# Kernel optimization log

Hardware: AMD Instinct MI355X
Metric: run time of the kernel (lower is better)

The kernel has to match this reference:

```python
import jax, jax.numpy as jnp
import numpy as np

EPS = 1e-16  # PyG softmax denominator epsilon


def segment_softmax(alpha, batch, num_segments):
    # alpha: (n,1); softmax within each bag (PyG-style: subtract segment max)
    m = jax.ops.segment_max(alpha, batch, num_segments=num_segments)
    e = jnp.exp(alpha - m[batch])
    s = jax.ops.segment_sum(e, batch, num_segments=num_segments)
    return e / (s[batch] + EPS)


def global_softmax_pooling(x, alpha, batch, num_segments):
    a = segment_softmax(alpha, batch, num_segments)
    return jax.ops.segment_sum(x * a, batch, num_segments=num_segments)  # (B,d)


def setup_inputs() -> dict:
    key = jax.random.key(0)
    k1, k2 = jax.random.split(key)
    n, d, B = 262144, 256, 512
    x = jax.random.normal(k1, (n, d), dtype=jnp.float32)
    batch = jnp.sort(jax.random.randint(k2, (n,), 0, B))
    return {"x": x, "batch": batch, "num_segments": B}


def reference(x, batch, num_segments):
    K = 3  # module default k
    alpha = jnp.zeros((x.shape[0], 1), dtype=x.dtype)
    for _ in range(K):  # small fixed iteration count
        z = global_softmax_pooling(x, alpha, batch, num_segments)  # (B,d)
        energy = jnp.sum(z * z, axis=1, keepdims=True)  # (B,1)
        z_squashed = jnp.sqrt(energy) / (1.0 + energy) * z  # (B,d)
        # alpha_i += <x_i, z_squashed[batch_i]> (vectorizes the per-bag mm loop)
        alpha = alpha + jnp.sum(x * z_squashed[batch], axis=1, keepdims=True)
    return global_softmax_pooling(x, alpha, batch, num_segments)
```

## Files before the change

### kernel.cpp

```cpp
#include <hip/hip_runtime.h>

#define D 256
#define CPS 4
#define TPB0 256
#define TPB1 1024
#define SLOTS 32
#define PSTR (D + 1)

__device__ __forceinline__ unsigned bfbits(float f) {
    unsigned u = __float_as_uint(f);
    return (u + 0x7fffu + ((u >> 16) & 1u)) >> 16;
}
__device__ __forceinline__ float bflo(unsigned u) { return __uint_as_float(u << 16); }
__device__ __forceinline__ float bfhi(unsigned u) { return __uint_as_float(u & 0xffff0000u); }

template<int USE_WS>
__global__ __launch_bounds__(TPB0, 8)
void pass0_k(const float* __restrict__ x, unsigned short* __restrict__ xb,
             const int* __restrict__ batch, float* __restrict__ part_out, int n)
{
    __shared__ float zp[8][D];
    __shared__ float sp[8];
    __shared__ int bnd[2];
    const int tid = threadIdx.x;
    const int s = blockIdx.x / CPS, k = blockIdx.x % CPS;
    const int hw = tid >> 5, l = tid & 31;

    if (tid < 2) {
        const int key = s + tid;
        int lo = 0, hi = n;
        while (lo < hi) { int mid = (lo + hi) >> 1; if (batch[mid] < key) lo = mid + 1; else hi = mid; }
        bnd[tid] = lo;
    }
    __syncthreads();
    const int start = bnd[0];
    const int cnt   = bnd[1] - start;
    const int csz   = (cnt + CPS - 1) / CPS;
    const int rbeg  = k * csz;
    const int rend  = min(cnt, rbeg + csz);

    float za[8] = {0,0,0,0,0,0,0,0};
    float s_acc = 0.f;
#pragma unroll 2
    for (int r = rbeg + hw; r < rend; r += 8) {
        const size_t boff = (size_t)(start + r) * D + l * 8;
        const float4 v0 = *(const float4*)(x + boff);
        const float4 v1 = *(const float4*)(x + boff + 4);
        if (USE_WS) {
            uint4 p;
            p.x = bfbits(v0.x) | (bfbits(v0.y) << 16);
            p.y = bfbits(v0.z) | (bfbits(v0.w) << 16);
            p.z = bfbits(v1.x) | (bfbits(v1.y) << 16);
            p.w = bfbits(v1.z) | (bfbits(v1.w) << 16);
            *(uint4*)(xb + boff) = p;
        }
        s_acc += 1.f;
        za[0] += v0.x; za[1] += v0.y; za[2] += v0.z; za[3] += v0.w;
        za[4] += v1.x; za[5] += v1.y; za[6] += v1.z; za[7] += v1.w;
    }
#pragma unroll
    for (int j = 0; j < 8; ++j) zp[hw][l * 8 + j] = za[j];
    if (l == 0) sp[hw] = s_acc;
    __syncthreads();
    float acc = 0.f;
#pragma unroll
    for (int h = 0; h < 8; ++h) acc += zp[h][tid];
    float* po = part_out + (size_t)(s * CPS + k) * PSTR;
    po[tid] = acc;
    if (tid == 0) {
        float st = 0.f;
#pragma unroll
        for (int h = 0; h < 8; ++h) st += sp[h];
        po[D] = st;
    }
}

template<int USE_WS>
__global__ __launch_bounds__(TPB1, 8)
void phases_k(const float* __restrict__ x, const unsigned short* __restrict__ xb,
              const int* __restrict__ batch,
              const float* __restrict__ part, float* __restrict__ out, int n)
{
    __shared__ float zp[SLOTS][D];
    __shared__ float sp[SLOTS];
    __shared__ float zs[D];
    __shared__ float red_e[16];
    __shared__ float red[2];
    __shared__ int bnd[2];
    const int tid  = threadIdx.x;
    const int s    = blockIdx.x;
    const int slot = tid >> 5;
    const int l    = tid & 31;
    const int wv   = tid >> 6;

    if (tid < 2) {
        const int key = s + tid;
        int lo = 0, hi = n;
        while (lo < hi) { int mid = (lo + hi) >> 1; if (batch[mid] < key) lo = mid + 1; else hi = mid; }
        bnd[tid] = lo;
    }
    __syncthreads();
    const int start = bnd[0];
    const int cnt   = bnd[1] - start;

    const float* pb = part + (size_t)s * CPS * PSTR;
    float z = 0.f;
    if (tid < D) {
#pragma unroll
        for (int kk = 0; kk < CPS; ++kk) z += pb[kk * PSTR + tid];
    }
    if (tid == 0) {
        float st = 0.f;
#pragma unroll
        for (int kk = 0; kk < CPS; ++kk) st += pb[kk * PSTR + D];
        red[0] = 1.f / (st + 1e-16f);
    }
    __syncthreads();
    z *= red[0];

    float Scol = 0.f;
    float zr[8];

    for (int ph = 1; ph <= 3; ++ph) {
        float e = (tid < D) ? z * z : 0.f;
#pragma unroll
        for (int o = 32; o; o >>= 1) e += __shfl_xor(e, o);
        if ((tid & 63) == 0) red_e[wv] = e;
        __syncthreads();
        if (tid == 0) {
            float E = 0.f;
#pragma unroll
            for (int h = 0; h < 16; ++h) E += red_e[h];
            red[1] = (E > 0.f) ? (sqrtf(E) / (1.f + E)) : 0.f;
        }
        __syncthreads();
        if (tid < D) { Scol += z * red[1]; zs[tid] = Scol; }
        __syncthreads();
#pragma unroll
        for (int j = 0; j < 8; ++j) zr[j] = zs[l * 8 + j];

        float za[8] = {0,0,0,0,0,0,0,0};
        float s_acc = 0.f;
        int r = slot;
        uint4 ucur = make_uint4(0,0,0,0);
        float4 c0 = {0,0,0,0}, c1 = {0,0,0,0};
        if (r < cnt) {
            const size_t o = (size_t)(start + r) * D + l * 8;
            if (USE_WS) ucur = *(const uint4*)(xb + o);
            else { c0 = *(const float4*)(x + o); c1 = *(const float4*)(x + o + 4); }
        }
        while (r < cnt) {
            const int rn = r + SLOTS;
            uint4 unxt = make_uint4(0,0,0,0);
            float4 n0 = {0,0,0,0}, n1 = {0,0,0,0};
            if (rn < cnt) {
                const size_t o = (size_t)(start + rn) * D + l * 8;
                if (USE_WS) unxt = *(const uint4*)(xb + o);
                else { n0 = *(const float4*)(x + o); n1 = *(const float4*)(x + o + 4); }
            }
            float xf[8];
            if (USE_WS) {
                xf[0]=bflo(ucur.x); xf[1]=bfhi(ucur.x); xf[2]=bflo(ucur.y); xf[3]=bfhi(ucur.y);
                xf[4]=bflo(ucur.z); xf[5]=bfhi(ucur.z); xf[6]=bflo(ucur.w); xf[7]=bfhi(ucur.w);
            } else {
                xf[0]=c0.x; xf[1]=c0.y; xf[2]=c0.z; xf[3]=c0.w;
                xf[4]=c1.x; xf[5]=c1.y; xf[6]=c1.z; xf[7]=c1.w;
            }
            float dt = 0.f;
#pragma unroll
            for (int j = 0; j < 8; ++j) dt += xf[j] * zr[j];
#pragma unroll
            for (int o = 16; o; o >>= 1) dt += __shfl_xor(dt, o);
            const float w = __expf(dt);
            s_acc += w;
#pragma unroll
            for (int j = 0; j < 8; ++j) za[j] += w * xf[j];
            ucur = unxt; c0 = n0; c1 = n1; r = rn;
        }

#pragma unroll
        for (int j = 0; j < 8; ++j) zp[slot][l * 8 + j] = za[j];
        if (l == 0) sp[slot] = s_acc;
        __syncthreads();
        z = 0.f;
        if (tid < D) {
#pragma unroll
            for (int h = 0; h < SLOTS; ++h) z += zp[h][tid];
        }
        if (tid == 0) {
            float st = 0.f;
#pragma unroll
            for (int h = 0; h < SLOTS; ++h) st += sp[h];
            red[0] = 1.f / (st + 1e-16f);
        }
        __syncthreads();
        z *= red[0];
    }

    if (tid < D) out[(size_t)s * D + tid] = z;
}

extern "C" void kernel_launch(void* const* d_in, const int* in_sizes, int n_in,
                              void* d_out, int out_size, void* d_ws, size_t ws_size,
                              hipStream_t stream) {
    const float* x   = (const float*)d_in[0];
    const int* batch = (const int*)d_in[1];
    float* out       = (float*)d_out;
    const int n = in_sizes[1];
    const int B = out_size / D;

    const size_t xb_bytes = (size_t)n * D * sizeof(unsigned short);
    const size_t pe = (size_t)B * CPS * PSTR;
    const bool use_ws = ws_size >= xb_bytes + pe * sizeof(float);

    unsigned short* xb = (unsigned short*)d_ws;
    float* pA = use_ws ? (float*)((char*)d_ws + xb_bytes) : (float*)d_ws;

    if (use_ws) {
        pass0_k<1><<<B * CPS, TPB0, 0, stream>>>(x, xb, batch, pA, n);
        phases_k<1><<<B, TPB1, 0, stream>>>(x, xb, batch, pA, out, n);
    } else {
        pass0_k<0><<<B * CPS, TPB0, 0, stream>>>(x, xb, batch, pA, n);
        phases_k<0><<<B, TPB1, 0, stream>>>(x, xb, batch, pA, out, n);
    }
}
```

Measured before the change: 143.2 us.

## Fuse bf16 conversion pass into the per-bag phases kernel

Merges the separate first pass (uniform mean and bf16 copy of x) into the single per-bag kernel, so one 1024-thread block per bag does all four pooling phases. This removes one kernel launch, the partial-sum buffer round trip, and the launch gap between the two kernels. The cross-slot reduction is also reworked into a two-level scheme using all threads, and the energy reduction is narrowed to the four waves that hold data. The trade-off is that the first pass now runs with only B blocks instead of B*4 smaller ones, which may lower parallelism for the heaviest fp32 read of x. Its first-phase loop also loses the unroll hint.

```diff
diff --git a/kernel.cpp b/kernel.cpp
--- a/kernel.cpp
+++ b/kernel.cpp
@@ -1,11 +1,8 @@
 #include <hip/hip_runtime.h>
 
 #define D 256
-#define CPS 4
-#define TPB0 256
-#define TPB1 1024
+#define TPB 1024
 #define SLOTS 32
-#define PSTR (D + 1)
 
 __device__ __forceinline__ unsigned bfbits(float f) {
     unsigned u = __float_as_uint(f);
@@ -15,83 +12,25 @@
 __device__ __forceinline__ float bfhi(unsigned u) { return __uint_as_float(u & 0xffff0000u); }
 
 template<int USE_WS>
-__global__ __launch_bounds__(TPB0, 8)
-void pass0_k(const float* __restrict__ x, unsigned short* __restrict__ xb,
-             const int* __restrict__ batch, float* __restrict__ part_out, int n)
-{
-    __shared__ float zp[8][D];
-    __shared__ float sp[8];
-    __shared__ int bnd[2];
-    const int tid = threadIdx.x;
-    const int s = blockIdx.x / CPS, k = blockIdx.x % CPS;
-    const int hw = tid >> 5, l = tid & 31;
-
-    if (tid < 2) {
-        const int key = s + tid;
-        int lo = 0, hi = n;
-        while (lo < hi) { int mid = (lo + hi) >> 1; if (batch[mid] < key) lo = mid + 1; else hi = mid; }
-        bnd[tid] = lo;
-    }
-    __syncthreads();
-    const int start = bnd[0];
-    const int cnt   = bnd[1] - start;
-    const int csz   = (cnt + CPS - 1) / CPS;
-    const int rbeg  = k * csz;
-    const int rend  = min(cnt, rbeg + csz);
-
-    float za[8] = {0,0,0,0,0,0,0,0};
-    float s_acc = 0.f;
-#pragma unroll 2
-    for (int r = rbeg + hw; r < rend; r += 8) {
-        const size_t boff = (size_t)(start + r) * D + l * 8;
-        const float4 v0 = *(const float4*)(x + boff);
-        const float4 v1 = *(const float4*)(x + boff + 4);
-        if (USE_WS) {
-            uint4 p;
-            p.x = bfbits(v0.x) | (bfbits(v0.y) << 16);
-            p.y = bfbits(v0.z) | (bfbits(v0.w) << 16);
-            p.z = bfbits(v1.x) | (bfbits(v1.y) << 16);
-            p.w = bfbits(v1.z) | (bfbits(v1.w) << 16);
-            *(uint4*)(xb + boff) = p;
-        }
-        s_acc += 1.f;
-        za[0] += v0.x; za[1] += v0.y; za[2] += v0.z; za[3] += v0.w;
-        za[4] += v1.x; za[5] += v1.y; za[6] += v1.z; za[7] += v1.w;
-    }
-#pragma unroll
-    for (int j = 0; j < 8; ++j) zp[hw][l * 8 + j] = za[j];
-    if (l == 0) sp[hw] = s_acc;
-    __syncthreads();
-    float acc = 0.f;
-#pragma unroll
-    for (int h = 0; h < 8; ++h) acc += zp[h][tid];
-    float* po = part_out + (size_t)(s * CPS + k) * PSTR;
-    po[tid] = acc;
-    if (tid == 0) {
-        float st = 0.f;
-#pragma unroll
-        for (int h = 0; h < 8; ++h) st += sp[h];
-        po[D] = st;
-    }
-}
-
-template<int USE_WS>
-__global__ __launch_bounds__(TPB1, 8)
-void phases_k(const float* __restrict__ x, const unsigned short* __restrict__ xb,
-              const int* __restrict__ batch,
-              const float* __restrict__ part, float* __restrict__ out, int n)
+__global__ __launch_bounds__(TPB, 8)
+void fused_k(const float* __restrict__ x, unsigned short* __restrict__ xb,
+             const int* __restrict__ batch, float* __restrict__ out, int n)
 {
     __shared__ float zp[SLOTS][D];
+    __shared__ float qp[4][D];
     __shared__ float sp[SLOTS];
     __shared__ float zs[D];
-    __shared__ float red_e[16];
     __shared__ float red[2];
+    __shared__ float red_e[4];
     __shared__ int bnd[2];
+
     const int tid  = threadIdx.x;
     const int s    = blockIdx.x;
     const int slot = tid >> 5;
     const int l    = tid & 31;
     const int wv   = tid >> 6;
+    const int q    = tid >> 8;
+    const int col  = tid & 255;
 
     if (tid < 2) {
         const int key = s + tid;
@@ -103,34 +42,101 @@
     const int start = bnd[0];
     const int cnt   = bnd[1] - start;
 
-    const float* pb = part + (size_t)s * CPS * PSTR;
+    float Scol = 0.f;
+    float zr[8] = {0,0,0,0,0,0,0,0};
     float z = 0.f;
-    if (tid < D) {
+
+    for (int ph = 0; ph < 4; ++ph) {
+        float za[8] = {0,0,0,0,0,0,0,0};
+        float s_acc = 0.f;
+
+        if (ph == 0) {
+            for (int r = slot; r < cnt; r += SLOTS) {
+                const size_t boff = (size_t)(start + r) * D + l * 8;
+                const float4 v0 = *(const float4*)(x + boff);
+                const float4 v1 = *(const float4*)(x + boff + 4);
+                if (USE_WS) {
+                    uint4 p;
+                    p.x = bfbits(v0.x) | (bfbits(v0.y) << 16);
+                    p.y = bfbits(v0.z) | (bfbits(v0.w) << 16);
+                    p.z = bfbits(v1.x) | (bfbits(v1.y) << 16);
+                    p.w = bfbits(v1.z) | (bfbits(v1.w) << 16);
+                    *(uint4*)(xb + boff) = p;
+                }
+                s_acc += 1.f;
+                za[0] += v0.x; za[1] += v0.y; za[2] += v0.z; za[3] += v0.w;
+                za[4] += v1.x; za[5] += v1.y; za[6] += v1.z; za[7] += v1.w;
+            }
+        } else {
+            int r = slot;
+            uint4 ucur = make_uint4(0,0,0,0);
+            float4 c0 = {0,0,0,0}, c1 = {0,0,0,0};
+            if (r < cnt) {
+                const size_t o = (size_t)(start + r) * D + l * 8;
+                if (USE_WS) ucur = *(const uint4*)(xb + o);
+                else { c0 = *(const float4*)(x + o); c1 = *(const float4*)(x + o + 4); }
+            }
+            while (r < cnt) {
+                const int rn = r + SLOTS;
+                uint4 unxt = make_uint4(0,0,0,0);
+                float4 n0 = {0,0,0,0}, n1 = {0,0,0,0};
+                if (rn < cnt) {
+                    const size_t o = (size_t)(start + rn) * D + l * 8;
+                    if (USE_WS) unxt = *(const uint4*)(xb + o);
+                    else { n0 = *(const float4*)(x + o); n1 = *(const float4*)(x + o + 4); }
+                }
+                float xf[8];
+                if (USE_WS) {
+                    xf[0]=bflo(ucur.x); xf[1]=bfhi(ucur.x); xf[2]=bflo(ucur.y); xf[3]=bfhi(ucur.y);
+                    xf[4]=bflo(ucur.z); xf[5]=bfhi(ucur.z); xf[6]=bflo(ucur.w); xf[7]=bfhi(ucur.w);
+                } else {
+                    xf[0]=c0.x; xf[1]=c0.y; xf[2]=c0.z; xf[3]=c0.w;
+                    xf[4]=c1.x; xf[5]=c1.y; xf[6]=c1.z; xf[7]=c1.w;
+                }
+                float dt = 0.f;
 #pragma unroll
-        for (int kk = 0; kk < CPS; ++kk) z += pb[kk * PSTR + tid];
-    }
-    if (tid == 0) {
-        float st = 0.f;
+                for (int j = 0; j < 8; ++j) dt += xf[j] * zr[j];
 #pragma unroll
-        for (int kk = 0; kk < CPS; ++kk) st += pb[kk * PSTR + D];
-        red[0] = 1.f / (st + 1e-16f);
-    }
-    __syncthreads();
-    z *= red[0];
+                for (int o = 16; o; o >>= 1) dt += __shfl_xor(dt, o);
+                const float w = __expf(dt);
+                s_acc += w;
+#pragma unroll
+                for (int j = 0; j < 8; ++j) za[j] += w * xf[j];
+                ucur = unxt; c0 = n0; c1 = n1; r = rn;
+            }
+        }
 
-    float Scol = 0.f;
-    float zr[8];
+#pragma unroll
+        for (int j = 0; j < 8; ++j) zp[slot][l * 8 + j] = za[j];
+        if (l == 0) sp[slot] = s_acc;
+        __syncthreads();
+        {
+            float p = 0.f;
+#pragma unroll
+            for (int h = 0; h < 8; ++h) p += zp[q * 8 + h][col];
+            qp[q][col] = p;
+            if (tid < 32) {
+                float st = sp[tid];
+#pragma unroll
+                for (int o = 16; o; o >>= 1) st += __shfl_xor(st, o);
+                if (tid == 0) red[0] = 1.f / (st + 1e-16f);
+            }
+        }
+        __syncthreads();
+        if (tid < D) z = (qp[0][tid] + qp[1][tid] + qp[2][tid] + qp[3][tid]) * red[0];
 
-    for (int ph = 1; ph <= 3; ++ph) {
+        if (ph == 3) {
+            if (tid < D) out[(size_t)s * D + tid] = z;
+            break;
+        }
+
         float e = (tid < D) ? z * z : 0.f;
 #pragma unroll
         for (int o = 32; o; o >>= 1) e += __shfl_xor(e, o);
-        if ((tid & 63) == 0) red_e[wv] = e;
+        if ((tid & 63) == 0 && wv < 4) red_e[wv] = e;
         __syncthreads();
         if (tid == 0) {
-            float E = 0.f;
-#pragma unroll
-            for (int h = 0; h < 16; ++h) E += red_e[h];
+            const float E = red_e[0] + red_e[1] + red_e[2] + red_e[3];
             red[1] = (E > 0.f) ? (sqrtf(E) / (1.f + E)) : 0.f;
         }
         __syncthreads();
@@ -138,66 +144,7 @@
         __syncthreads();
 #pragma unroll
         for (int j = 0; j < 8; ++j) zr[j] = zs[l * 8 + j];
-
-        float za[8] = {0,0,0,0,0,0,0,0};
-        float s_acc = 0.f;
-        int r = slot;
-        uint4 ucur = make_uint4(0,0,0,0);
-        float4 c0 = {0,0,0,0}, c1 = {0,0,0,0};
-        if (r < cnt) {
-            const size_t o = (size_t)(start + r) * D + l * 8;
-            if (USE_WS) ucur = *(const uint4*)(xb + o);
-            else { c0 = *(const float4*)(x + o); c1 = *(const float4*)(x + o + 4); }
-        }
-        while (r < cnt) {
-            const int rn = r + SLOTS;
-            uint4 unxt = make_uint4(0,0,0,0);
-            float4 n0 = {0,0,0,0}, n1 = {0,0,0,0};
-            if (rn < cnt) {
-                const size_t o = (size_t)(start + rn) * D + l * 8;
-                if (USE_WS) unxt = *(const uint4*)(xb + o);
-                else { n0 = *(const float4*)(x + o); n1 = *(const float4*)(x + o + 4); }
-            }
-            float xf[8];
-            if (USE_WS) {
-                xf[0]=bflo(ucur.x); xf[1]=bfhi(ucur.x); xf[2]=bflo(ucur.y); xf[3]=bfhi(ucur.y);
-                xf[4]=bflo(ucur.z); xf[5]=bfhi(ucur.z); xf[6]=bflo(ucur.w); xf[7]=bfhi(ucur.w);
-            } else {
-                xf[0]=c0.x; xf[1]=c0.y; xf[2]=c0.z; xf[3]=c0.w;
-                xf[4]=c1.x; xf[5]=c1.y; xf[6]=c1.z; xf[7]=c1.w;
-            }
-            float dt = 0.f;
-#pragma unroll
-            for (int j = 0; j < 8; ++j) dt += xf[j] * zr[j];
-#pragma unroll
-            for (int o = 16; o; o >>= 1) dt += __shfl_xor(dt, o);
-            const float w = __expf(dt);
-            s_acc += w;
-#pragma unroll
-            for (int j = 0; j < 8; ++j) za[j] += w * xf[j];
-            ucur = unxt; c0 = n0; c1 = n1; r = rn;
-        }
-
-#pragma unroll
-        for (int j = 0; j < 8; ++j) zp[slot][l * 8 + j] = za[j];
-        if (l == 0) sp[slot] = s_acc;
-        __syncthreads();
-        z = 0.f;
-        if (tid < D) {
-#pragma unroll
-            for (int h = 0; h < SLOTS; ++h) z += zp[h][tid];
-        }
-        if (tid == 0) {
-            float st = 0.f;
-#pragma unroll
-            for (int h = 0; h < SLOTS; ++h) st += sp[h];
-            red[0] = 1.f / (st + 1e-16f);
-        }
-        __syncthreads();
-        z *= red[0];
     }
-
-    if (tid < D) out[(size_t)s * D + tid] = z;
 }
 
 extern "C" void kernel_launch(void* const* d_in, const int* in_sizes, int n_in,
@@ -210,17 +157,9 @@
     const int B = out_size / D;
 
     const size_t xb_bytes = (size_t)n * D * sizeof(unsigned short);
-    const size_t pe = (size_t)B * CPS * PSTR;
-    const bool use_ws = ws_size >= xb_bytes + pe * sizeof(float);
+    const bool use_ws = ws_size >= xb_bytes;
+    unsigned short* xb = (unsigned short*)d_ws;
 
-    unsigned short* xb = (unsigned short*)d_ws;
-    float* pA = use_ws ? (float*)((char*)d_ws + xb_bytes) : (float*)d_ws;
-
-    if (use_ws) {
-        pass0_k<1><<<B * CPS, TPB0, 0, stream>>>(x, xb, batch, pA, n);
-        phases_k<1><<<B, TPB1, 0, stream>>>(x, xb, batch, pA, out, n);
-    } else {
-        pass0_k<0><<<B * CPS, TPB0, 0, stream>>>(x, xb, batch, pA, n);
-        phases_k<0><<<B, TPB1, 0, stream>>>(x, xb, batch, pA, out, n);
-    }
+    if (use_ws) fused_k<1><<<B, TPB, 0, stream>>>(x, xb, batch, out, n);
+    else        fused_k<0><<<B, TPB, 0, stream>>>(x, xb, batch, out, n);
 }
```

After: 146.6 us. 2.4% more time.
